# Optimization experiments

Hardware: AMD Instinct MI355X
Metric: run time of the kernel (lower is better)

Reference implementation:

```python
import jax, jax.numpy as jnp
import numpy as np

DIM = 256
NUM_HEADS = 4
HEAD_DIM = DIM // NUM_HEADS
EPS = 1e-5


def setup_inputs() -> dict:
    key = jax.random.key(0)
    ks = jax.random.split(key, 8)
    B, N, C = 8, 2048, DIM
    s = 0.02
    return {
        "x": jax.random.normal(ks[0], (B, N, C), jnp.float32),
        "qkv_w": jax.random.normal(ks[1], (C, 3 * C), jnp.float32) * s,
        "qkv_b": jnp.zeros((3 * C,), jnp.float32),
        "proj_w": jax.random.normal(ks[2], (C, C), jnp.float32) * s,
        "proj_b": jnp.zeros((C,), jnp.float32),
        "ln1_g": jnp.ones((C,), jnp.float32),
        "ln1_b": jnp.zeros((C,), jnp.float32),
        "ln2_g": jnp.ones((C,), jnp.float32),
        "ln2_b": jnp.zeros((C,), jnp.float32),
        "mlp_w1": jax.random.normal(ks[3], (C, 2 * C), jnp.float32) * s,
        "mlp_b1": jnp.zeros((2 * C,), jnp.float32),
        "mlp_w2": jax.random.normal(ks[4], (2 * C, C), jnp.float32) * s,
        "mlp_b2": jnp.zeros((C,), jnp.float32),
    }


def _layernorm(x, g, b):
    mu = jnp.mean(x, axis=-1, keepdims=True)
    var = jnp.mean(jnp.square(x - mu), axis=-1, keepdims=True)
    return (x - mu) * jax.lax.rsqrt(var + EPS) * g + b


def reference(x, qkv_w, qkv_b, proj_w, proj_b, ln1_g, ln1_b, ln2_g, ln2_b,
              mlp_w1, mlp_b1, mlp_w2, mlp_b2):
    B, N, C = x.shape
    H, D = NUM_HEADS, HEAD_DIM
    shortcut = x
    h = _layernorm(x, ln1_g, ln1_b)
    qkv = (h @ qkv_w + qkv_b).reshape(B, N, 3, H, D)
    q = qkv[:, :, 0].transpose(0, 2, 1, 3)  # [B,H,N,D]
    k = qkv[:, :, 1].transpose(0, 2, 1, 3)
    v = qkv[:, :, 2].transpose(0, 2, 1, 3)
    attn = jnp.einsum('bhnd,bhmd->bhnm', q, k) * (D ** -0.5)
    attn = jax.nn.softmax(attn, axis=-1)  # dropout = identity (eval mode)
    o = jnp.einsum('bhnm,bhmd->bhnd', attn, v)
    o = o.transpose(0, 2, 1, 3).reshape(B, N, C)
    x = o @ proj_w + proj_b + shortcut
    h2 = _layernorm(x, ln2_g, ln2_b)
    mlp = jax.nn.gelu(h2 @ mlp_w1 + mlp_b1, approximate=False) @ mlp_w2 + mlp_b2
    return x + mlp
```

## Files before the change

### kernel.cpp

```cpp
#include <hip/hip_runtime.h>

typedef __bf16 bf16;
typedef __bf16 bf16x8 __attribute__((ext_vector_type(8)));
typedef __bf16 bf16x4 __attribute__((ext_vector_type(4)));
typedef float  f32x4  __attribute__((ext_vector_type(4)));
typedef unsigned u32x2 __attribute__((ext_vector_type(2)));

typedef __attribute__((address_space(1))) const void GASV;
typedef __attribute__((address_space(3))) void LASV;

__device__ __forceinline__ void gload16(const void* g, void* l) {
  __builtin_amdgcn_global_load_lds((GASV*)g, (LASV*)l, 16, 0, 0);
}

__global__ __launch_bounds__(256) void wconv_t(const float* __restrict__ in,
                                               bf16* __restrict__ out,
                                               int lgK, int Cin, int total) {
  int idx = blockIdx.x * 256 + threadIdx.x;
  if (idx >= total) return;
  int K = 1 << lgK;
  int k = idx & (K - 1);
  int n = idx >> lgK;
  out[idx] = (bf16)in[(size_t)k * Cin + n];
}

__global__ __launch_bounds__(256) void ln_fwd(const float* __restrict__ x,
                                              const float* __restrict__ gam,
                                              const float* __restrict__ bet,
                                              bf16* __restrict__ out) {
  const int lane = threadIdx.x & 63;
  const int w = threadIdx.x >> 6;
  const size_t row = (size_t)blockIdx.x * 4 + w;
  const float4 v = *(const float4*)(x + row * 256 + lane * 4);
  float s1 = v.x + v.y + v.z + v.w;
  float s2 = v.x * v.x + v.y * v.y + v.z * v.z + v.w * v.w;
#pragma unroll
  for (int m = 1; m < 64; m <<= 1) {
    s1 += __shfl_xor(s1, m);
    s2 += __shfl_xor(s2, m);
  }
  const float mu = s1 * (1.0f / 256.0f);
  const float var = s2 * (1.0f / 256.0f) - mu * mu;
  const float rs = rsqrtf(var + 1e-5f);
  const float4 g4 = *(const float4*)(gam + lane * 4);
  const float4 b4 = *(const float4*)(bet + lane * 4);
  bf16x4 o;
  o[0] = (bf16)((v.x - mu) * rs * g4.x + b4.x);
  o[1] = (bf16)((v.y - mu) * rs * g4.y + b4.y);
  o[2] = (bf16)((v.z - mu) * rs * g4.z + b4.z);
  o[3] = (bf16)((v.w - mu) * rs * g4.w + b4.w);
  *(bf16x4*)(out + row * 256 + lane * 4) = o;
}

template <int EPI>
__global__ __launch_bounds__(256) void gemm_bt(const bf16* __restrict__ A,
                                               const bf16* __restrict__ Bt,
                                               const float* __restrict__ bias,
                                               const float* __restrict__ res,
                                               void* __restrict__ outp,
                                               int M, int N, int K) {
  __shared__ bf16 Al[2][8192];
  __shared__ bf16 Bl[2][8192];
  const int tid = threadIdx.x;
  const int lane = tid & 63;
  const int wid = tid >> 6;
  const int wm = wid >> 1, wn = wid & 1;
  const int nbm = M >> 7;
  const int bm = (int)blockIdx.x % nbm;
  const int bn = (int)blockIdx.x / nbm;
  const int m0 = bm << 7, n0 = bn << 7;
  const int nk = K >> 6;

  f32x4 acc[4][4];
#pragma unroll
  for (int i = 0; i < 4; ++i)
#pragma unroll
    for (int j = 0; j < 4; ++j) acc[i][j] = (f32x4){0.f, 0.f, 0.f, 0.f};

  auto stage = [&](int t, int s) {
    const int k0 = t << 6;
#pragma unroll
    for (int p = 0; p < 4; ++p) {
      const int idx = p * 4096 + tid * 16;
      const int row = idx >> 7;
      const int colb = idx & 127;
      gload16((const char*)(A + ((size_t)(m0 + row) * K + k0)) + colb,
              (char*)&Al[s][0] + p * 4096 + ((tid >> 6) << 10));
      gload16((const char*)(Bt + ((size_t)(n0 + row) * K + k0)) + colb,
              (char*)&Bl[s][0] + p * 4096 + ((tid >> 6) << 10));
    }
  };

  stage(0, 0);
  asm volatile("s_waitcnt vmcnt(0)" ::: "memory");
  __syncthreads();

  for (int t = 0; t < nk; ++t) {
    if (t + 1 < nk) stage(t + 1, (t + 1) & 1);
    const bf16* pa = &Al[t & 1][0] + (wm * 64 + (lane & 15)) * 64 + ((lane >> 4) << 3);
    const bf16* pb = &Bl[t & 1][0] + (wn * 64 + (lane & 15)) * 64 + ((lane >> 4) << 3);
    bf16x8 av[4][2], bv[4][2];
#pragma unroll
    for (int f = 0; f < 4; ++f)
#pragma unroll
      for (int ks = 0; ks < 2; ++ks) {
        av[f][ks] = *(const bf16x8*)(pa + f * 1024 + ks * 32);
        bv[f][ks] = *(const bf16x8*)(pb + f * 1024 + ks * 32);
      }
    __builtin_amdgcn_s_setprio(1);
#pragma unroll
    for (int fm = 0; fm < 4; ++fm)
#pragma unroll
      for (int fn = 0; fn < 4; ++fn) {
        acc[fm][fn] = __builtin_amdgcn_mfma_f32_16x16x32_bf16(av[fm][0], bv[fn][0], acc[fm][fn], 0, 0, 0);
        acc[fm][fn] = __builtin_amdgcn_mfma_f32_16x16x32_bf16(av[fm][1], bv[fn][1], acc[fm][fn], 0, 0, 0);
      }
    __builtin_amdgcn_s_setprio(0);
    asm volatile("s_waitcnt vmcnt(0)" ::: "memory");
    __syncthreads();
  }

#pragma unroll
  for (int fm = 0; fm < 4; ++fm)
#pragma unroll
    for (int fn = 0; fn < 4; ++fn) {
      const int r0 = m0 + wm * 64 + fm * 16 + ((lane >> 4) << 2);
      const int c = n0 + wn * 64 + fn * 16 + (lane & 15);
#pragma unroll
      for (int j = 0; j < 4; ++j) {
        const int r = r0 + j;
        const float v = acc[fm][fn][j];
        if constexpr (EPI == 0) {
          ((bf16*)outp)[(size_t)r * N + c] = (bf16)(v + bias[c]);
        } else if constexpr (EPI == 1) {
          ((bf16*)outp)[(size_t)r * 2048 + ((size_t)(c >> 11)) * 524288 + (c & 2047)] =
              (bf16)(v + bias[r]);
        } else if constexpr (EPI == 2) {
          ((float*)outp)[(size_t)r * N + c] = v + bias[c] + res[(size_t)r * N + c];
        } else {
          const float u = v + bias[c];
          ((bf16*)outp)[(size_t)r * N + c] = (bf16)(u * 0.5f * (1.0f + erff(u * 0.70710678118f)));
        }
      }
    }
}

__global__ __launch_bounds__(256) void attn_fwd(const bf16* __restrict__ qk,
                                                const bf16* __restrict__ vT,
                                                bf16* __restrict__ ob) {
  __shared__ bf16 Kl[2][4096];
  __shared__ bf16 Vl[2][4096];
  __shared__ bf16 Pl[4][1024];
  const int tid = threadIdx.x;
  const int lane = tid & 63;
  const int w = tid >> 6;
  const int g = lane >> 4;
  const int qi = lane & 15;
  const int bh = blockIdx.x & 31;
  const int qt = blockIdx.x >> 5;
  const int b = bh >> 2, h = bh & 3;

  const size_t qrow = (size_t)b * 2048 + qt * 64 + w * 16 + qi;
  const bf16* qp = qk + qrow * 512 + h * 64 + g * 8;
  const bf16x8 qf0 = *(const bf16x8*)qp;
  const bf16x8 qf1 = *(const bf16x8*)(qp + 32);

  float mrun = 0.0f, lsum = 0.0f;
  f32x4 o[4];
#pragma unroll
  for (int i = 0; i < 4; ++i) o[i] = (f32x4){0.f, 0.f, 0.f, 0.f};

  const char* kbase = (const char*)qk + ((size_t)b * 2048) * 1024 + 512 + h * 128;
  const char* vbase = (const char*)vT + (size_t)bh * 262144;
  constexpr float CEXP = 0.125f * 1.44269504088896340736f;
  constexpr float THR = 8.0f / CEXP;

  int koff[2], voff[2];
#pragma unroll
  for (int i = 0; i < 2; ++i) {
    const int fk = i * 2 + (w >> 1);
    const int half = w & 1;
    koff[i] = (fk * 16 + qi) * 1024 + half * 64 + g * 16;
    voff[i] = (fk * 16 + qi) * 4096 + half * 64 + g * 16;
  }
  char* const pw = (char*)&Pl[w][0];
  int paddr[4];
#pragma unroll
  for (int fk = 0; fk < 4; ++fk)
    paddr[fk] = (fk >> 1) * 1024 + ((fk & 1) * 2 + (g >> 1)) * 256 + qi * 16 + ((g & 1) * 2) * 4;
  const char* const pr = (const char*)&Pl[w][0] + lane * 16;

  auto stage = [&](int t, int s) {
    const size_t kt = (size_t)t * 65536;
    const size_t vt = (size_t)t * 128;
#pragma unroll
    for (int i = 0; i < 2; ++i) {
      gload16(kbase + kt + koff[i], (char*)&Kl[s][0] + i * 4096 + w * 1024);
      gload16(vbase + vt + voff[i], (char*)&Vl[s][0] + i * 4096 + w * 1024);
    }
  };

  stage(0, 0);
  asm volatile("s_waitcnt vmcnt(0)" ::: "memory");
  __syncthreads();

  for (int t = 0; t < 32; ++t) {
    if (t < 31) stage(t + 1, (t + 1) & 1);
    const int s = t & 1;
    const char* kb = (const char*)&Kl[s][0] + lane * 16;
    f32x4 st[4];
    __builtin_amdgcn_s_setprio(1);
#pragma unroll
    for (int fk = 0; fk < 4; ++fk) {
      const bf16x8 k0 = *(const bf16x8*)(kb + fk * 2048);
      const bf16x8 k1 = *(const bf16x8*)(kb + fk * 2048 + 1024);
      f32x4 z = (f32x4){0.f, 0.f, 0.f, 0.f};
      st[fk] = __builtin_amdgcn_mfma_f32_16x16x32_bf16(k0, qf0, z, 0, 0, 0);
      st[fk] = __builtin_amdgcn_mfma_f32_16x16x32_bf16(k1, qf1, st[fk], 0, 0, 0);
    }
    __builtin_amdgcn_s_setprio(0);
    float pmax = st[0][0];
#pragma unroll
    for (int fk = 0; fk < 4; ++fk)
#pragma unroll
      for (int j = 0; j < 4; ++j) pmax = fmaxf(pmax, st[fk][j]);
    if (!__all(pmax <= mrun + THR)) {
      float mt = fmaxf(pmax, __shfl_xor(pmax, 16));
      mt = fmaxf(mt, __shfl_xor(mt, 32));
      const float mnew = fmaxf(mrun, mt);
      const float alpha = exp2f(CEXP * (mrun - mnew));
      lsum *= alpha;
#pragma unroll
      for (int fd = 0; fd < 4; ++fd)
#pragma unroll
        for (int j = 0; j < 4; ++j) o[fd][j] *= alpha;
      mrun = mnew;
    }
    const float negcm = -CEXP * mrun;
    float ts = 0.f;
    unsigned pk[8];
#pragma unroll
    for (int fk = 0; fk < 4; ++fk)
#pragma unroll
      for (int jp = 0; jp < 2; ++jp) {
        const float p0 = exp2f(fmaf(st[fk][2 * jp], CEXP, negcm));
        const float p1 = exp2f(fmaf(st[fk][2 * jp + 1], CEXP, negcm));
        ts += p0 + p1;
        union { bf16 h2[2]; unsigned u; } cv;
        cv.h2[0] = (bf16)p0;
        cv.h2[1] = (bf16)p1;
        pk[fk * 2 + jp] = cv.u;
      }
    ts += __shfl_xor(ts, 16);
    ts += __shfl_xor(ts, 32);
    lsum += ts;
#pragma unroll
    for (int fk = 0; fk < 4; ++fk) {
      u32x2 pr2;
      pr2[0] = pk[fk * 2];
      pr2[1] = pk[fk * 2 + 1];
      *(u32x2*)(pw + paddr[fk]) = pr2;
    }
    const bf16x8 pa0 = *(const bf16x8*)(pr);
    const bf16x8 pa1 = *(const bf16x8*)(pr + 1024);
    const char* vb = (const char*)&Vl[s][0] + lane * 16;
    __builtin_amdgcn_s_setprio(1);
#pragma unroll
    for (int fd = 0; fd < 4; ++fd) {
      const bf16x8 v0 = *(const bf16x8*)(vb + fd * 2048);
      const bf16x8 v1 = *(const bf16x8*)(vb + fd * 2048 + 1024);
      o[fd] = __builtin_amdgcn_mfma_f32_16x16x32_bf16(v0, pa0, o[fd], 0, 0, 0);
      o[fd] = __builtin_amdgcn_mfma_f32_16x16x32_bf16(v1, pa1, o[fd], 0, 0, 0);
    }
    __builtin_amdgcn_s_setprio(0);
    asm volatile("s_waitcnt vmcnt(0)" ::: "memory");
    __syncthreads();
  }

  const float inv = 1.0f / lsum;
  bf16* const orow = ob + qrow * 256 + h * 64 + g * 4;
#pragma unroll
  for (int fd = 0; fd < 4; ++fd) {
    bf16x4 ov;
#pragma unroll
    for (int j = 0; j < 4; ++j) ov[j] = (bf16)(o[fd][j] * inv);
    *(bf16x4*)(orow + fd * 16) = ov;
  }
}

extern "C" void kernel_launch(void* const* d_in, const int* in_sizes, int n_in,
                              void* d_out, int out_size, void* d_ws, size_t ws_size,
                              hipStream_t stream) {
  const float* x      = (const float*)d_in[0];
  const float* qkv_w  = (const float*)d_in[1];
  const float* qkv_b  = (const float*)d_in[2];
  const float* proj_w = (const float*)d_in[3];
  const float* proj_b = (const float*)d_in[4];
  const float* ln1_g  = (const float*)d_in[5];
  const float* ln1_b  = (const float*)d_in[6];
  const float* ln2_g  = (const float*)d_in[7];
  const float* ln2_b  = (const float*)d_in[8];
  const float* mlp_w1 = (const float*)d_in[9];
  const float* mlp_b1 = (const float*)d_in[10];
  const float* mlp_w2 = (const float*)d_in[11];
  const float* mlp_b2 = (const float*)d_in[12];
  float* out = (float*)d_out;

  char* ws = (char*)d_ws;
  bf16* Wtqkv = (bf16*)(ws);
  bf16* WtP   = (bf16*)(ws + 393216);
  bf16* Wt1   = (bf16*)(ws + 524288);
  bf16* Wt2   = (bf16*)(ws + 786432);
  bf16* h     = (bf16*)(ws + 1048576);
  bf16* qkb   = (bf16*)(ws + 9437184);
  bf16* vT    = (bf16*)(ws + 26214400);
  bf16* obuf  = (bf16*)(ws + 34603008);
  float* x2   = (float*)(ws + 42991616);
  bf16* a1 = qkb;
  bf16* h2 = h;

  wconv_t<<<768, 256, 0, stream>>>(qkv_w, Wtqkv, 8, 768, 196608);
  wconv_t<<<256, 256, 0, stream>>>(proj_w, WtP, 8, 256, 65536);
  wconv_t<<<512, 256, 0, stream>>>(mlp_w1, Wt1, 8, 512, 131072);
  wconv_t<<<512, 256, 0, stream>>>(mlp_w2, Wt2, 9, 256, 131072);

  ln_fwd<<<4096, 256, 0, stream>>>(x, ln1_g, ln1_b, h);
  gemm_bt<0><<<512, 256, 0, stream>>>(h, Wtqkv, qkv_b, nullptr, qkb, 16384, 512, 256);
  gemm_bt<1><<<256, 256, 0, stream>>>(Wtqkv + 512 * 256, h, qkv_b + 512, nullptr, vT, 256, 16384, 256);
  attn_fwd<<<1024, 256, 0, stream>>>(qkb, vT, obuf);
  gemm_bt<2><<<256, 256, 0, stream>>>(obuf, WtP, proj_b, x, x2, 16384, 256, 256);
  ln_fwd<<<4096, 256, 0, stream>>>(x2, ln2_g, ln2_b, h2);
  gemm_bt<3><<<512, 256, 0, stream>>>(h2, Wt1, mlp_b1, nullptr, a1, 16384, 512, 256);
  gemm_bt<2><<<256, 256, 0, stream>>>(a1, Wt2, mlp_b2, x2, out, 16384, 256, 512);
}
```

Measured before the change: 179.1 us.

## Double attention query tile per wave, triple-buffer K/V, fuse weight conversions

```diff
diff --git a/kernel.cpp b/kernel.cpp
--- a/kernel.cpp
+++ b/kernel.cpp
@@ -13,15 +13,28 @@
   __builtin_amdgcn_global_load_lds((GASV*)g, (LASV*)l, 16, 0, 0);
 }
 
-__global__ __launch_bounds__(256) void wconv_t(const float* __restrict__ in,
-                                               bf16* __restrict__ out,
-                                               int lgK, int Cin, int total) {
-  int idx = blockIdx.x * 256 + threadIdx.x;
-  if (idx >= total) return;
-  int K = 1 << lgK;
-  int k = idx & (K - 1);
-  int n = idx >> lgK;
-  out[idx] = (bf16)in[(size_t)k * Cin + n];
+__global__ __launch_bounds__(256) void wconv_all(const float* __restrict__ qkv_w,
+                                                 const float* __restrict__ proj_w,
+                                                 const float* __restrict__ w1,
+                                                 const float* __restrict__ w2,
+                                                 bf16* __restrict__ Wtqkv,
+                                                 bf16* __restrict__ WtP,
+                                                 bf16* __restrict__ Wt1,
+                                                 bf16* __restrict__ Wt2) {
+  const int idx = blockIdx.x * 256 + threadIdx.x;
+  if (idx < 196608) {
+    const int k = idx & 255, n = idx >> 8;
+    Wtqkv[idx] = (bf16)qkv_w[k * 768 + n];
+  } else if (idx < 262144) {
+    const int i = idx - 196608, k = i & 255, n = i >> 8;
+    WtP[i] = (bf16)proj_w[k * 256 + n];
+  } else if (idx < 393216) {
+    const int i = idx - 262144, k = i & 255, n = i >> 8;
+    Wt1[i] = (bf16)w1[k * 512 + n];
+  } else {
+    const int i = idx - 393216, k = i & 511, n = i >> 9;
+    Wt2[i] = (bf16)w2[k * 256 + n];
+  }
 }
 
 __global__ __launch_bounds__(256) void ln_fwd(const float* __restrict__ x,
@@ -148,9 +161,9 @@
 __global__ __launch_bounds__(256) void attn_fwd(const bf16* __restrict__ qk,
                                                 const bf16* __restrict__ vT,
                                                 bf16* __restrict__ ob) {
-  __shared__ bf16 Kl[2][4096];
-  __shared__ bf16 Vl[2][4096];
-  __shared__ bf16 Pl[4][1024];
+  __shared__ bf16 Kl[3][4096];
+  __shared__ bf16 Vl[3][4096];
+  __shared__ bf16 Pl[4][2048];
   const int tid = threadIdx.x;
   const int lane = tid & 63;
   const int w = tid >> 6;
@@ -160,131 +173,175 @@
   const int qt = blockIdx.x >> 5;
   const int b = bh >> 2, h = bh & 3;
 
-  const size_t qrow = (size_t)b * 2048 + qt * 64 + w * 16 + qi;
-  const bf16* qp = qk + qrow * 512 + h * 64 + g * 8;
-  const bf16x8 qf0 = *(const bf16x8*)qp;
-  const bf16x8 qf1 = *(const bf16x8*)(qp + 32);
-
-  float mrun = 0.0f, lsum = 0.0f;
-  f32x4 o[4];
-#pragma unroll
-  for (int i = 0; i < 4; ++i) o[i] = (f32x4){0.f, 0.f, 0.f, 0.f};
+  const size_t qrow0 = (size_t)b * 2048 + qt * 128 + w * 32 + qi;
+  bf16x8 qf[2][2];
+#pragma unroll
+  for (int f = 0; f < 2; ++f) {
+    const bf16* qp = qk + (qrow0 + f * 16) * 512 + h * 64 + g * 8;
+    qf[f][0] = *(const bf16x8*)qp;
+    qf[f][1] = *(const bf16x8*)(qp + 32);
+  }
+
+  float mrun[2] = {0.f, 0.f};
+  float lsum[2] = {0.f, 0.f};
+  f32x4 o[4][2];
+#pragma unroll
+  for (int i = 0; i < 4; ++i)
+#pragma unroll
+    for (int f = 0; f < 2; ++f) o[i][f] = (f32x4){0.f, 0.f, 0.f, 0.f};
+
+  constexpr float CEXP = 0.125f * 1.44269504088896340736f;
+  constexpr float THR = 8.0f / CEXP;
 
   const char* kbase = (const char*)qk + ((size_t)b * 2048) * 1024 + 512 + h * 128;
   const char* vbase = (const char*)vT + (size_t)bh * 262144;
-  constexpr float CEXP = 0.125f * 1.44269504088896340736f;
-  constexpr float THR = 8.0f / CEXP;
-
-  int koff[2], voff[2];
+  const char* ks[2];
+  const char* vs[2];
 #pragma unroll
   for (int i = 0; i < 2; ++i) {
     const int fk = i * 2 + (w >> 1);
     const int half = w & 1;
-    koff[i] = (fk * 16 + qi) * 1024 + half * 64 + g * 16;
-    voff[i] = (fk * 16 + qi) * 4096 + half * 64 + g * 16;
+    ks[i] = kbase + (fk * 16 + qi) * 1024 + half * 64 + g * 16;
+    vs[i] = vbase + (size_t)(fk * 16 + qi) * 4096 + half * 64 + g * 16;
   }
   char* const pw = (char*)&Pl[w][0];
   int paddr[4];
 #pragma unroll
   for (int fk = 0; fk < 4; ++fk)
-    paddr[fk] = (fk >> 1) * 1024 + ((fk & 1) * 2 + (g >> 1)) * 256 + qi * 16 + ((g & 1) * 2) * 4;
-  const char* const pr = (const char*)&Pl[w][0] + lane * 16;
-
-  auto stage = [&](int t, int s) {
-    const size_t kt = (size_t)t * 65536;
-    const size_t vt = (size_t)t * 128;
-#pragma unroll
-    for (int i = 0; i < 2; ++i) {
-      gload16(kbase + kt + koff[i], (char*)&Kl[s][0] + i * 4096 + w * 1024);
-      gload16(vbase + vt + voff[i], (char*)&Vl[s][0] + i * 4096 + w * 1024);
-    }
+    paddr[fk] = (fk >> 1) * 2048 + ((fk & 1) * 2 + (g >> 1)) * 256 + qi * 16 + (g & 1) * 8;
+  const char* const prd = (const char*)&Pl[w][0] + lane * 16;
+
+  auto stage = [&](int slot) {
+    char* kd = (char*)&Kl[0][0] + slot * 8192 + w * 1024;
+    char* vd = (char*)&Vl[0][0] + slot * 8192 + w * 1024;
+    gload16(ks[0], kd);
+    gload16(ks[1], kd + 4096);
+    gload16(vs[0], vd);
+    gload16(vs[1], vd + 4096);
+    ks[0] += 65536; ks[1] += 65536;
+    vs[0] += 128;   vs[1] += 128;
   };
 
-  stage(0, 0);
-  asm volatile("s_waitcnt vmcnt(0)" ::: "memory");
-  __syncthreads();
-
+  stage(0);
+  stage(1);
+  asm volatile("s_waitcnt vmcnt(4)" ::: "memory");
+  __builtin_amdgcn_s_barrier();
+
+  int slot = 0, slot2 = 2;
   for (int t = 0; t < 32; ++t) {
-    if (t < 31) stage(t + 1, (t + 1) & 1);
-    const int s = t & 1;
-    const char* kb = (const char*)&Kl[s][0] + lane * 16;
-    f32x4 st[4];
+    if (t < 30) stage(slot2);
+    const char* kb = (const char*)&Kl[0][0] + slot * 8192 + lane * 16;
+    f32x4 st[4][2];
     __builtin_amdgcn_s_setprio(1);
 #pragma unroll
     for (int fk = 0; fk < 4; ++fk) {
       const bf16x8 k0 = *(const bf16x8*)(kb + fk * 2048);
       const bf16x8 k1 = *(const bf16x8*)(kb + fk * 2048 + 1024);
-      f32x4 z = (f32x4){0.f, 0.f, 0.f, 0.f};
-      st[fk] = __builtin_amdgcn_mfma_f32_16x16x32_bf16(k0, qf0, z, 0, 0, 0);
-      st[fk] = __builtin_amdgcn_mfma_f32_16x16x32_bf16(k1, qf1, st[fk], 0, 0, 0);
+#pragma unroll
+      for (int f = 0; f < 2; ++f) {
+        f32x4 z = (f32x4){0.f, 0.f, 0.f, 0.f};
+        st[fk][f] = __builtin_amdgcn_mfma_f32_16x16x32_bf16(k0, qf[f][0], z, 0, 0, 0);
+        st[fk][f] = __builtin_amdgcn_mfma_f32_16x16x32_bf16(k1, qf[f][1], st[fk][f], 0, 0, 0);
+      }
     }
     __builtin_amdgcn_s_setprio(0);
-    float pmax = st[0][0];
-#pragma unroll
-    for (int fk = 0; fk < 4; ++fk)
-#pragma unroll
-      for (int j = 0; j < 4; ++j) pmax = fmaxf(pmax, st[fk][j]);
-    if (!__all(pmax <= mrun + THR)) {
-      float mt = fmaxf(pmax, __shfl_xor(pmax, 16));
-      mt = fmaxf(mt, __shfl_xor(mt, 32));
-      const float mnew = fmaxf(mrun, mt);
-      const float alpha = exp2f(CEXP * (mrun - mnew));
-      lsum *= alpha;
-#pragma unroll
-      for (int fd = 0; fd < 4; ++fd)
-#pragma unroll
-        for (int j = 0; j < 4; ++j) o[fd][j] *= alpha;
-      mrun = mnew;
-    }
-    const float negcm = -CEXP * mrun;
-    float ts = 0.f;
-    unsigned pk[8];
-#pragma unroll
-    for (int fk = 0; fk < 4; ++fk)
-#pragma unroll
-      for (int jp = 0; jp < 2; ++jp) {
-        const float p0 = exp2f(fmaf(st[fk][2 * jp], CEXP, negcm));
-        const float p1 = exp2f(fmaf(st[fk][2 * jp + 1], CEXP, negcm));
-        ts += p0 + p1;
-        union { bf16 h2[2]; unsigned u; } cv;
-        cv.h2[0] = (bf16)p0;
-        cv.h2[1] = (bf16)p1;
-        pk[fk * 2 + jp] = cv.u;
-      }
-    ts += __shfl_xor(ts, 16);
-    ts += __shfl_xor(ts, 32);
-    lsum += ts;
+    float pmax[2];
+#pragma unroll
+    for (int f = 0; f < 2; ++f) {
+      float m0 = fmaxf(fmaxf(st[0][f][0], st[0][f][1]), fmaxf(st[0][f][2], st[0][f][3]));
+      float m1 = fmaxf(fmaxf(st[1][f][0], st[1][f][1]), fmaxf(st[1][f][2], st[1][f][3]));
+      float m2 = fmaxf(fmaxf(st[2][f][0], st[2][f][1]), fmaxf(st[2][f][2], st[2][f][3]));
+      float m3 = fmaxf(fmaxf(st[3][f][0], st[3][f][1]), fmaxf(st[3][f][2], st[3][f][3]));
+      pmax[f] = fmaxf(fmaxf(m0, m1), fmaxf(m2, m3));
+    }
+    if (!__all(pmax[0] <= mrun[0] + THR && pmax[1] <= mrun[1] + THR)) {
+#pragma unroll
+      for (int f = 0; f < 2; ++f) {
+        float mt = fmaxf(pmax[f], __shfl_xor(pmax[f], 16));
+        mt = fmaxf(mt, __shfl_xor(mt, 32));
+        const float mnew = fmaxf(mrun[f], mt);
+        const float alpha = exp2f(CEXP * (mrun[f] - mnew));
+        lsum[f] *= alpha;
+#pragma unroll
+        for (int fd = 0; fd < 4; ++fd)
+#pragma unroll
+          for (int j = 0; j < 4; ++j) o[fd][f][j] *= alpha;
+        mrun[f] = mnew;
+      }
+    }
+    unsigned pk[4][2][2];
+#pragma unroll
+    for (int f = 0; f < 2; ++f) {
+      const float negcm = -CEXP * mrun[f];
+      float ts = 0.f;
+#pragma unroll
+      for (int fk = 0; fk < 4; ++fk)
+#pragma unroll
+        for (int jp = 0; jp < 2; ++jp) {
+          const float p0 = exp2f(fmaf(st[fk][f][2 * jp], CEXP, negcm));
+          const float p1 = exp2f(fmaf(st[fk][f][2 * jp + 1], CEXP, negcm));
+          ts += p0 + p1;
+          union { bf16 h2[2]; unsigned u; } cv;
+          cv.h2[0] = (bf16)p0;
+          cv.h2[1] = (bf16)p1;
+          pk[fk][f][jp] = cv.u;
+        }
+      lsum[f] += ts;
+    }
 #pragma unroll
     for (int fk = 0; fk < 4; ++fk) {
-      u32x2 pr2;
-      pr2[0] = pk[fk * 2];
-      pr2[1] = pk[fk * 2 + 1];
-      *(u32x2*)(pw + paddr[fk]) = pr2;
-    }
-    const bf16x8 pa0 = *(const bf16x8*)(pr);
-    const bf16x8 pa1 = *(const bf16x8*)(pr + 1024);
-    const char* vb = (const char*)&Vl[s][0] + lane * 16;
+      u32x2 w0, w1;
+      w0[0] = pk[fk][0][0]; w0[1] = pk[fk][0][1];
+      w1[0] = pk[fk][1][0]; w1[1] = pk[fk][1][1];
+      *(u32x2*)(pw + paddr[fk]) = w0;
+      *(u32x2*)(pw + paddr[fk] + 1024) = w1;
+    }
+    bf16x8 pa[2][2];
+#pragma unroll
+    for (int f = 0; f < 2; ++f)
+#pragma unroll
+      for (int ksl = 0; ksl < 2; ++ksl)
+        pa[f][ksl] = *(const bf16x8*)(prd + ksl * 2048 + f * 1024);
+    const char* vb = (const char*)&Vl[0][0] + slot * 8192 + lane * 16;
     __builtin_amdgcn_s_setprio(1);
 #pragma unroll
     for (int fd = 0; fd < 4; ++fd) {
       const bf16x8 v0 = *(const bf16x8*)(vb + fd * 2048);
       const bf16x8 v1 = *(const bf16x8*)(vb + fd * 2048 + 1024);
-      o[fd] = __builtin_amdgcn_mfma_f32_16x16x32_bf16(v0, pa0, o[fd], 0, 0, 0);
-      o[fd] = __builtin_amdgcn_mfma_f32_16x16x32_bf16(v1, pa1, o[fd], 0, 0, 0);
+#pragma unroll
+      for (int f = 0; f < 2; ++f) {
+        o[fd][f] = __builtin_amdgcn_mfma_f32_16x16x32_bf16(v0, pa[f][0], o[fd][f], 0, 0, 0);
+        o[fd][f] = __builtin_amdgcn_mfma_f32_16x16x32_bf16(v1, pa[f][1], o[fd][f], 0, 0, 0);
+      }
     }
     __builtin_amdgcn_s_setprio(0);
-    asm volatile("s_waitcnt vmcnt(0)" ::: "memory");
-    __syncthreads();
-  }
-
-  const float inv = 1.0f / lsum;
-  bf16* const orow = ob + qrow * 256 + h * 64 + g * 4;
-#pragma unroll
-  for (int fd = 0; fd < 4; ++fd) {
-    bf16x4 ov;
-#pragma unroll
-    for (int j = 0; j < 4; ++j) ov[j] = (bf16)(o[fd][j] * inv);
-    *(bf16x4*)(orow + fd * 16) = ov;
+    if (t < 30) {
+      asm volatile("s_waitcnt vmcnt(4)" ::: "memory");
+    } else {
+      asm volatile("s_waitcnt vmcnt(0)" ::: "memory");
+    }
+    __builtin_amdgcn_s_barrier();
+    slot = (slot == 2) ? 0 : slot + 1;
+    slot2 = (slot2 == 2) ? 0 : slot2 + 1;
+  }
+
+#pragma unroll
+  for (int f = 0; f < 2; ++f) {
+    float l = lsum[f];
+    l += __shfl_xor(l, 16);
+    l += __shfl_xor(l, 32);
+    lsum[f] = 1.0f / l;
+  }
+#pragma unroll
+  for (int f = 0; f < 2; ++f) {
+    bf16* const orow = ob + (qrow0 + f * 16) * 256 + h * 64 + g * 4;
+#pragma unroll
+    for (int fd = 0; fd < 4; ++fd) {
+      bf16x4 ov;
+#pragma unroll
+      for (int j = 0; j < 4; ++j) ov[j] = (bf16)(o[fd][f][j] * lsum[f]);
+      *(bf16x4*)(orow + fd * 16) = ov;
+    }
   }
 }
 
@@ -319,15 +376,12 @@
   bf16* a1 = qkb;
   bf16* h2 = h;
 
-  wconv_t<<<768, 256, 0, stream>>>(qkv_w, Wtqkv, 8, 768, 196608);
-  wconv_t<<<256, 256, 0, stream>>>(proj_w, WtP, 8, 256, 65536);
-  wconv_t<<<512, 256, 0, stream>>>(mlp_w1, Wt1, 8, 512, 131072);
-  wconv_t<<<512, 256, 0, stream>>>(mlp_w2, Wt2, 9, 256, 131072);
+  wconv_all<<<2048, 256, 0, stream>>>(qkv_w, proj_w, mlp_w1, mlp_w2, Wtqkv, WtP, Wt1, Wt2);
 
   ln_fwd<<<4096, 256, 0, stream>>>(x, ln1_g, ln1_b, h);
   gemm_bt<0><<<512, 256, 0, stream>>>(h, Wtqkv, qkv_b, nullptr, qkb, 16384, 512, 256);
   gemm_bt<1><<<256, 256, 0, stream>>>(Wtqkv + 512 * 256, h, qkv_b + 512, nullptr, vT, 256, 16384, 256);
-  attn_fwd<<<1024, 256, 0, stream>>>(qkb, vT, obuf);
+  attn_fwd<<<512, 256, 0, stream>>>(qkb, vT, obuf);
   gemm_bt<2><<<256, 256, 0, stream>>>(obuf, WtP, proj_b, x, x2, 16384, 256, 256);
   ln_fwd<<<4096, 256, 0, stream>>>(x2, ln2_g, ln2_b, h2);
   gemm_bt<3><<<512, 256, 0, stream>>>(h2, Wt1, mlp_b1, nullptr, a1, 16384, 512, 256);
```

Result: faster. 171.4 us (-4.3%).
